# Performance work log

Hardware: AMD Instinct MI355X
Metric: run time of the kernel (lower is better)

Reference implementation:

```python
import jax, jax.numpy as jnp
import numpy as np

BATCH, SEQ, DMODEL, NSTATE = 4, 2048, 1024, 16


def setup_inputs() -> dict:
    key = jax.random.key(0)
    ks = jax.random.split(key, 6)
    def lin_w(k, out_d, in_d):
        # torch Linear default init scale ~ 1/sqrt(in_d)
        return jax.random.uniform(k, (out_d, in_d), jnp.float32, -1.0, 1.0) / np.sqrt(in_d).astype(np.float32)
    return {
        "x": jax.random.normal(ks[0], (BATCH, SEQ, DMODEL), jnp.float32),
        "W1": lin_w(ks[1], DMODEL, DMODEL), "b1": jnp.zeros((DMODEL,), jnp.float32),
        "W2": lin_w(ks[2], NSTATE, DMODEL), "b2": jnp.zeros((NSTATE,), jnp.float32),
        "W3": lin_w(ks[3], NSTATE, DMODEL), "b3": jnp.zeros((NSTATE,), jnp.float32),
        # A: xavier_uniform over (d_model, state_size)
        "A": jax.random.uniform(ks[4], (DMODEL, NSTATE), jnp.float32, -1.0, 1.0) * np.sqrt(6.0 / (DMODEL + NSTATE)).astype(np.float32),
    }


def reference(x, W1, b1, W2, b2, W3, b3, A):
    # Projections (bld -> bln / bld)
    Bmat = x @ W2.T + b2                      # (b, l, n)
    Cmat = x @ W3.T + b3                      # (b, l, n)
    delta = jax.nn.softplus(x @ W1.T + b1)    # (b, l, d)
    # Original math (flag=0 path):
    #   dB[b,l,d,n] = delta[b,l,d] * B[b,l,n]
    #   dA = exp(einsum('bld,dn->bldn', delta, A))  -- multiplied by a zeros h, so it
    #        contributes nothing to the output (dead math; A receives zero grad).
    #   h  = dA * 0 + x[...,None] * dB
    #   y  = einsum('bln,bldn->bld', C, h)
    # This reduces exactly to: y = x * delta * sum_n(B * C)
    bc = jnp.einsum('bln,bln->bl', Bmat, Cmat)  # (b, l)
    y = x * delta * bc[..., None]               # (b, l, d)
    return y
```

## Files before the change

kernel.cpp:

```cpp
#include <hip/hip_runtime.h>
#include <hip/hip_bf16.h>
#include <cmath>

#define BATCH 4
#define SEQ 2048
#define DM 1024
#define NS 16
#define M_ROWS (BATCH * SEQ)

typedef short bf16x8 __attribute__((ext_vector_type(8)));
typedef short bf16x4 __attribute__((ext_vector_type(4)));
typedef float f32x4 __attribute__((ext_vector_type(4)));

__device__ __forceinline__ short f2bf(float f) {
    union { float f; unsigned u; } a; a.f = f;
    unsigned u = a.u;
    return (short)((u + 0x7fffu + ((u >> 16) & 1u)) >> 16);
}
__device__ __forceinline__ float bf2f(unsigned short s) {
    union { unsigned u; float f; } a; a.u = ((unsigned)s) << 16;
    return a.f;
}

#define LDS_CAST(p) ((__attribute__((address_space(3))) unsigned*)(p))
#define GLB_CAST(p) ((const __attribute__((address_space(1))) unsigned*)(p))

__global__ void __launch_bounds__(256) convert_all(
    const float* __restrict__ x,  const float* __restrict__ W1,
    const float* __restrict__ W2, const float* __restrict__ W3,
    short* __restrict__ xb, short* __restrict__ W1b, short* __restrict__ Wcb)
{
    const int b = blockIdx.x;
    const int t = threadIdx.x;
    const float4* src; bf16x4* dst; int qbase;
    if (b < 2048)      { src = (const float4*)x;  dst = (bf16x4*)xb;  qbase = b * 1024; }
    else if (b < 2304) { src = (const float4*)W1; dst = (bf16x4*)W1b; qbase = (b - 2048) * 1024; }
    else if (b < 2308) { src = (const float4*)W2; dst = (bf16x4*)Wcb; qbase = (b - 2304) * 1024; }
    else               { src = (const float4*)W3; dst = (bf16x4*)(Wcb + NS * DM); qbase = (b - 2308) * 1024; }
    #pragma unroll
    for (int i = 0; i < 4; i++) {
        int q = qbase + i * 256 + t;
        float4 v = src[q];
        bf16x4 s;
        s.x = f2bf(v.x); s.y = f2bf(v.y); s.z = f2bf(v.z); s.w = f2bf(v.w);
        dst[q] = s;
    }
}

__global__ void __launch_bounds__(256) gemm_fused(
    const short* __restrict__ xb, const short* __restrict__ W1b,
    const short* __restrict__ Wcb, const float* __restrict__ b1,
    const float* __restrict__ b2,  const float* __restrict__ b3,
    float* __restrict__ out)
{
    __shared__ short As[64][64];
    __shared__ short Bs[128][64];
    __shared__ short Wcs[32][64];
    __shared__ float bcs[64];

    const int n0 = blockIdx.x * 128;
    const int m0 = blockIdx.y * 64;
    const int t = threadIdx.x;
    const int lane = t & 63;
    const int w = t >> 6;
    const int wm = (w >> 1) * 32;
    const int wn = (w & 1) * 64;
    const int lm = lane & 15;
    const int quad = lane >> 4;

    const int srow = t >> 3;
    const int schunk = t & 7;
    const int gch = (schunk ^ (srow & 7)) * 8;

    const short* pa0 = xb  + (size_t)(m0 + srow)      * DM + gch;
    const short* pa1 = xb  + (size_t)(m0 + 32 + srow) * DM + gch;
    const short* pb0 = W1b + (size_t)(n0 + srow)      * DM + gch;
    const short* pb1 = W1b + (size_t)(n0 + 32 + srow) * DM + gch;
    const short* pb2 = W1b + (size_t)(n0 + 64 + srow) * DM + gch;
    const short* pb3 = W1b + (size_t)(n0 + 96 + srow) * DM + gch;
    const short* pw  = Wcb + (size_t)srow             * DM + gch;

    f32x4 acc[2][4] = {};
    f32x4 abc[2] = {};

    #pragma unroll
    for (int kk = 0; kk < 16; kk++) {
        const int ke = kk * 64;
        __builtin_amdgcn_global_load_lds(GLB_CAST(pa0 + ke), LDS_CAST(&As[srow][schunk * 8]),      16, 0, 0);
        __builtin_amdgcn_global_load_lds(GLB_CAST(pa1 + ke), LDS_CAST(&As[32 + srow][schunk * 8]), 16, 0, 0);
        __builtin_amdgcn_global_load_lds(GLB_CAST(pb0 + ke), LDS_CAST(&Bs[srow][schunk * 8]),      16, 0, 0);
        __builtin_amdgcn_global_load_lds(GLB_CAST(pb1 + ke), LDS_CAST(&Bs[32 + srow][schunk * 8]), 16, 0, 0);
        __builtin_amdgcn_global_load_lds(GLB_CAST(pb2 + ke), LDS_CAST(&Bs[64 + srow][schunk * 8]), 16, 0, 0);
        __builtin_amdgcn_global_load_lds(GLB_CAST(pb3 + ke), LDS_CAST(&Bs[96 + srow][schunk * 8]), 16, 0, 0);
        __builtin_amdgcn_global_load_lds(GLB_CAST(pw  + ke), LDS_CAST(&Wcs[srow][schunk * 8]),     16, 0, 0);
        __syncthreads();

        #pragma unroll
        for (int ks = 0; ks < 2; ks++) {
            const int g = ks * 4 + quad;
            bf16x8 af[2], bfv[4], wcv[2], ab;
            #pragma unroll
            for (int i = 0; i < 2; i++) {
                int r = wm + i * 16 + lm;
                af[i] = *(const bf16x8*)&As[r][(g ^ (r & 7)) * 8];
            }
            #pragma unroll
            for (int j = 0; j < 4; j++) {
                int r = wn + j * 16 + lm;
                bfv[j] = *(const bf16x8*)&Bs[r][(g ^ (r & 7)) * 8];
            }
            {
                int rb = w * 16 + lm;
                ab = *(const bf16x8*)&As[rb][(g ^ (rb & 7)) * 8];
            }
            #pragma unroll
            for (int jj = 0; jj < 2; jj++) {
                int r = jj * 16 + lm;
                wcv[jj] = *(const bf16x8*)&Wcs[r][(g ^ (r & 7)) * 8];
            }
            #pragma unroll
            for (int i = 0; i < 2; i++)
                #pragma unroll
                for (int j = 0; j < 4; j++)
                    acc[i][j] = __builtin_amdgcn_mfma_f32_16x16x32_bf16(
                        af[i], bfv[j], acc[i][j], 0, 0, 0);
            #pragma unroll
            for (int jj = 0; jj < 2; jj++)
                abc[jj] = __builtin_amdgcn_mfma_f32_16x16x32_bf16(
                    ab, wcv[jj], abc[jj], 0, 0, 0);
        }
        __syncthreads();
    }

    float bb2 = b2[lm], bb3 = b3[lm];
    #pragma unroll
    for (int r = 0; r < 4; r++) {
        float p = (abc[0][r] + bb2) * (abc[1][r] + bb3);
        p += __shfl_xor(p, 1);
        p += __shfl_xor(p, 2);
        p += __shfl_xor(p, 4);
        p += __shfl_xor(p, 8);
        if (lm == 0) bcs[w * 16 + quad * 4 + r] = p;
    }
    __syncthreads();

    const unsigned short* xbu = (const unsigned short*)xb;
    float b1v[4];
    #pragma unroll
    for (int j = 0; j < 4; j++) b1v[j] = b1[n0 + wn + j * 16 + lm];

    #pragma unroll
    for (int i = 0; i < 2; i++) {
        #pragma unroll
        for (int r = 0; r < 4; r++) {
            int lrow = wm + i * 16 + quad * 4 + r;
            int gm = m0 + lrow;
            float bcv = bcs[lrow];
            const unsigned short* xrow = xbu + (size_t)gm * DM + n0 + wn + lm;
            float* orow = out + (size_t)gm * DM + n0 + wn + lm;
            #pragma unroll
            for (int j = 0; j < 4; j++) {
                float z = acc[i][j][r] + b1v[j];
                float az = __builtin_fabsf(z);
                float sp = fmaxf(z, 0.f) + __logf(1.f + __expf(-az));
                orow[j * 16] = bf2f(xrow[j * 16]) * sp * bcv;
            }
        }
    }
}

extern "C" void kernel_launch(void* const* d_in, const int* in_sizes, int n_in,
                              void* d_out, int out_size, void* d_ws, size_t ws_size,
                              hipStream_t stream) {
    const float* x  = (const float*)d_in[0];
    const float* W1 = (const float*)d_in[1];
    const float* b1 = (const float*)d_in[2];
    const float* W2 = (const float*)d_in[3];
    const float* b2 = (const float*)d_in[4];
    const float* W3 = (const float*)d_in[5];
    const float* b3 = (const float*)d_in[6];
    float* out = (float*)d_out;

    char* ws = (char*)d_ws;
    short* xb  = (short*)(ws);
    short* W1b = (short*)(ws + (size_t)16 * 1024 * 1024);
    short* Wcb = (short*)(ws + (size_t)18 * 1024 * 1024);

    convert_all<<<2312, 256, 0, stream>>>(x, W1, W2, W3, xb, W1b, Wcb);

    dim3 grid(DM / 128, M_ROWS / 64);
    gemm_fused<<<grid, 256, 0, stream>>>(xb, W1b, Wcb, b1, b2, b3, out);
}
```

Measured before the change: 128.0 us.

## Double-buffer LDS tiles with K=32 steps to overlap loads with MFMA

Splits the shared-memory tiles into two buffers of K=32 and prefetches the next K slice while MFMAs run on the current one, using a single barrier per iteration. The swizzle changes to a 4-chunk XOR pattern to match the narrower rows. The aim is to hide global-to-LDS latency behind compute. In exchange it doubles the number of iterations and barriers, and each barrier now waits on the in-flight prefetch, which may limit the overlap.

```diff
diff --git a/kernel.cpp b/kernel.cpp
--- a/kernel.cpp
+++ b/kernel.cpp
@@ -53,9 +53,9 @@
     const float* __restrict__ b2,  const float* __restrict__ b3,
     float* __restrict__ out)
 {
-    __shared__ short As[64][64];
-    __shared__ short Bs[128][64];
-    __shared__ short Wcs[32][64];
+    __shared__ short As[2][64][32];
+    __shared__ short Bs[2][128][32];
+    __shared__ short Wcs[2][32][32];
     __shared__ float bcs[64];
 
     const int n0 = blockIdx.x * 128;
@@ -68,67 +68,64 @@
     const int lm = lane & 15;
     const int quad = lane >> 4;
 
-    const int srow = t >> 3;
-    const int schunk = t & 7;
-    const int gch = (schunk ^ (srow & 7)) * 8;
+    const int srow = t >> 2;
+    const int sch  = t & 3;
+    const int gchS = (sch ^ (srow & 3)) * 8;
+    const int wrow = t >> 2;
+    const int gchW = (sch ^ (wrow & 3)) * 8;
 
-    const short* pa0 = xb  + (size_t)(m0 + srow)      * DM + gch;
-    const short* pa1 = xb  + (size_t)(m0 + 32 + srow) * DM + gch;
-    const short* pb0 = W1b + (size_t)(n0 + srow)      * DM + gch;
-    const short* pb1 = W1b + (size_t)(n0 + 32 + srow) * DM + gch;
-    const short* pb2 = W1b + (size_t)(n0 + 64 + srow) * DM + gch;
-    const short* pb3 = W1b + (size_t)(n0 + 96 + srow) * DM + gch;
-    const short* pw  = Wcb + (size_t)srow             * DM + gch;
+    const short* pa  = xb  + (size_t)(m0 + srow) * DM + gchS;
+    const short* pb0 = W1b + (size_t)(n0 + srow) * DM + gchS;
+    const short* pb1 = pb0 + (size_t)64 * DM;
+    const short* pw  = Wcb + (size_t)wrow * DM + gchW;
+
+    const int cs = ((quad ^ (lm & 3))) * 8;
 
     f32x4 acc[2][4] = {};
     f32x4 abc[2] = {};
 
+    __builtin_amdgcn_global_load_lds(GLB_CAST(pa),  LDS_CAST(&As[0][srow][sch * 8]),      16, 0, 0);
+    __builtin_amdgcn_global_load_lds(GLB_CAST(pb0), LDS_CAST(&Bs[0][srow][sch * 8]),      16, 0, 0);
+    __builtin_amdgcn_global_load_lds(GLB_CAST(pb1), LDS_CAST(&Bs[0][64 + srow][sch * 8]), 16, 0, 0);
+    if (t < 128)
+        __builtin_amdgcn_global_load_lds(GLB_CAST(pw), LDS_CAST(&Wcs[0][wrow][sch * 8]),  16, 0, 0);
+    __syncthreads();
+
     #pragma unroll
-    for (int kk = 0; kk < 16; kk++) {
-        const int ke = kk * 64;
-        __builtin_amdgcn_global_load_lds(GLB_CAST(pa0 + ke), LDS_CAST(&As[srow][schunk * 8]),      16, 0, 0);
-        __builtin_amdgcn_global_load_lds(GLB_CAST(pa1 + ke), LDS_CAST(&As[32 + srow][schunk * 8]), 16, 0, 0);
-        __builtin_amdgcn_global_load_lds(GLB_CAST(pb0 + ke), LDS_CAST(&Bs[srow][schunk * 8]),      16, 0, 0);
-        __builtin_amdgcn_global_load_lds(GLB_CAST(pb1 + ke), LDS_CAST(&Bs[32 + srow][schunk * 8]), 16, 0, 0);
-        __builtin_amdgcn_global_load_lds(GLB_CAST(pb2 + ke), LDS_CAST(&Bs[64 + srow][schunk * 8]), 16, 0, 0);
-        __builtin_amdgcn_global_load_lds(GLB_CAST(pb3 + ke), LDS_CAST(&Bs[96 + srow][schunk * 8]), 16, 0, 0);
-        __builtin_amdgcn_global_load_lds(GLB_CAST(pw  + ke), LDS_CAST(&Wcs[srow][schunk * 8]),     16, 0, 0);
-        __syncthreads();
+    for (int kk = 0; kk < 32; kk++) {
+        const int p = kk & 1;
+        if (kk < 31) {
+            const int ke = (kk + 1) * 32;
+            __builtin_amdgcn_global_load_lds(GLB_CAST(pa  + ke), LDS_CAST(&As[1 - p][srow][sch * 8]),      16, 0, 0);
+            __builtin_amdgcn_global_load_lds(GLB_CAST(pb0 + ke), LDS_CAST(&Bs[1 - p][srow][sch * 8]),      16, 0, 0);
+            __builtin_amdgcn_global_load_lds(GLB_CAST(pb1 + ke), LDS_CAST(&Bs[1 - p][64 + srow][sch * 8]), 16, 0, 0);
+            if (t < 128)
+                __builtin_amdgcn_global_load_lds(GLB_CAST(pw + ke), LDS_CAST(&Wcs[1 - p][wrow][sch * 8]),  16, 0, 0);
+        }
+
+        bf16x8 af[2], bfv[4], wcv[2], ab;
+        #pragma unroll
+        for (int i = 0; i < 2; i++)
+            af[i] = *(const bf16x8*)&As[p][wm + i * 16 + lm][cs];
+        #pragma unroll
+        for (int j = 0; j < 4; j++)
+            bfv[j] = *(const bf16x8*)&Bs[p][wn + j * 16 + lm][cs];
+        ab = *(const bf16x8*)&As[p][w * 16 + lm][cs];
+        #pragma unroll
+        for (int jj = 0; jj < 2; jj++)
+            wcv[jj] = *(const bf16x8*)&Wcs[p][jj * 16 + lm][cs];
 
         #pragma unroll
-        for (int ks = 0; ks < 2; ks++) {
-            const int g = ks * 4 + quad;
-            bf16x8 af[2], bfv[4], wcv[2], ab;
+        for (int i = 0; i < 2; i++)
             #pragma unroll
-            for (int i = 0; i < 2; i++) {
-                int r = wm + i * 16 + lm;
-                af[i] = *(const bf16x8*)&As[r][(g ^ (r & 7)) * 8];
-            }
-            #pragma unroll
-            for (int j = 0; j < 4; j++) {
-                int r = wn + j * 16 + lm;
-                bfv[j] = *(const bf16x8*)&Bs[r][(g ^ (r & 7)) * 8];
-            }
-            {
-                int rb = w * 16 + lm;
-                ab = *(const bf16x8*)&As[rb][(g ^ (rb & 7)) * 8];
-            }
-            #pragma unroll
-            for (int jj = 0; jj < 2; jj++) {
-                int r = jj * 16 + lm;
-                wcv[jj] = *(const bf16x8*)&Wcs[r][(g ^ (r & 7)) * 8];
-            }
-            #pragma unroll
-            for (int i = 0; i < 2; i++)
-                #pragma unroll
-                for (int j = 0; j < 4; j++)
-                    acc[i][j] = __builtin_amdgcn_mfma_f32_16x16x32_bf16(
-                        af[i], bfv[j], acc[i][j], 0, 0, 0);
-            #pragma unroll
-            for (int jj = 0; jj < 2; jj++)
-                abc[jj] = __builtin_amdgcn_mfma_f32_16x16x32_bf16(
-                    ab, wcv[jj], abc[jj], 0, 0, 0);
-        }
+            for (int j = 0; j < 4; j++)
+                acc[i][j] = __builtin_amdgcn_mfma_f32_16x16x32_bf16(
+                    af[i], bfv[j], acc[i][j], 0, 0, 0);
+        #pragma unroll
+        for (int jj = 0; jj < 2; jj++)
+            abc[jj] = __builtin_amdgcn_mfma_f32_16x16x32_bf16(
+                ab, wcv[jj], abc[jj], 0, 0, 0);
+
         __syncthreads();
     }
 
```

New measurement: 148.7 us. 1.16x slower.

## Enlarge GEMM tile to 128x128 with 4x4 MFMA fragments per wave

Applied to the files above, without the earlier changes.

Doubles the M tile from 64 to 128 rows, so each wave computes a 64x64 output region using 4x4 MFMA accumulators. The B/C projection now reuses the A fragments already loaded for the main GEMM instead of doing a separate LDS read. The goal is higher arithmetic intensity and less global and LDS traffic per output. In exchange there are more registers per thread, more LDS, and half as many blocks (512), which reduces occupancy and wave-level parallelism.

```diff
diff --git a/kernel.cpp b/kernel.cpp
--- a/kernel.cpp
+++ b/kernel.cpp
@@ -53,94 +53,88 @@
     const float* __restrict__ b2,  const float* __restrict__ b3,
     float* __restrict__ out)
 {
-    __shared__ short As[64][64];
+    __shared__ short As[128][64];
     __shared__ short Bs[128][64];
     __shared__ short Wcs[32][64];
-    __shared__ float bcs[64];
+    __shared__ float bcs[128];
 
     const int n0 = blockIdx.x * 128;
-    const int m0 = blockIdx.y * 64;
+    const int m0 = blockIdx.y * 128;
     const int t = threadIdx.x;
     const int lane = t & 63;
     const int w = t >> 6;
-    const int wm = (w >> 1) * 32;
+    const int wm = (w >> 1) * 64;
     const int wn = (w & 1) * 64;
     const int lm = lane & 15;
     const int quad = lane >> 4;
 
-    const int srow = t >> 3;
-    const int schunk = t & 7;
-    const int gch = (schunk ^ (srow & 7)) * 8;
+    const int sr  = t >> 3;
+    const int sc  = t & 7;
+    const int gch = (sc ^ (sr & 7)) * 8;
 
-    const short* pa0 = xb  + (size_t)(m0 + srow)      * DM + gch;
-    const short* pa1 = xb  + (size_t)(m0 + 32 + srow) * DM + gch;
-    const short* pb0 = W1b + (size_t)(n0 + srow)      * DM + gch;
-    const short* pb1 = W1b + (size_t)(n0 + 32 + srow) * DM + gch;
-    const short* pb2 = W1b + (size_t)(n0 + 64 + srow) * DM + gch;
-    const short* pb3 = W1b + (size_t)(n0 + 96 + srow) * DM + gch;
-    const short* pw  = Wcb + (size_t)srow             * DM + gch;
+    const short* pa = xb  + (size_t)(m0 + sr) * DM + gch;
+    const short* pb = W1b + (size_t)(n0 + sr) * DM + gch;
+    const short* pw = Wcb + (size_t)sr        * DM + gch;
 
-    f32x4 acc[2][4] = {};
-    f32x4 abc[2] = {};
+    f32x4 acc[4][4] = {};
+    f32x4 abc[2][2] = {};
 
     #pragma unroll
     for (int kk = 0; kk < 16; kk++) {
         const int ke = kk * 64;
-        __builtin_amdgcn_global_load_lds(GLB_CAST(pa0 + ke), LDS_CAST(&As[srow][schunk * 8]),      16, 0, 0);
-        __builtin_amdgcn_global_load_lds(GLB_CAST(pa1 + ke), LDS_CAST(&As[32 + srow][schunk * 8]), 16, 0, 0);
-        __builtin_amdgcn_global_load_lds(GLB_CAST(pb0 + ke), LDS_CAST(&Bs[srow][schunk * 8]),      16, 0, 0);
-        __builtin_amdgcn_global_load_lds(GLB_CAST(pb1 + ke), LDS_CAST(&Bs[32 + srow][schunk * 8]), 16, 0, 0);
-        __builtin_amdgcn_global_load_lds(GLB_CAST(pb2 + ke), LDS_CAST(&Bs[64 + srow][schunk * 8]), 16, 0, 0);
-        __builtin_amdgcn_global_load_lds(GLB_CAST(pb3 + ke), LDS_CAST(&Bs[96 + srow][schunk * 8]), 16, 0, 0);
-        __builtin_amdgcn_global_load_lds(GLB_CAST(pw  + ke), LDS_CAST(&Wcs[srow][schunk * 8]),     16, 0, 0);
+        #pragma unroll
+        for (int u = 0; u < 4; u++) {
+            __builtin_amdgcn_global_load_lds(GLB_CAST(pa + (size_t)u * 32 * DM + ke),
+                LDS_CAST(&As[u * 32 + sr][sc * 8]), 16, 0, 0);
+            __builtin_amdgcn_global_load_lds(GLB_CAST(pb + (size_t)u * 32 * DM + ke),
+                LDS_CAST(&Bs[u * 32 + sr][sc * 8]), 16, 0, 0);
+        }
+        __builtin_amdgcn_global_load_lds(GLB_CAST(pw + ke),
+            LDS_CAST(&Wcs[sr][sc * 8]), 16, 0, 0);
         __syncthreads();
 
         #pragma unroll
         for (int ks = 0; ks < 2; ks++) {
-            const int g = ks * 4 + quad;
-            bf16x8 af[2], bfv[4], wcv[2], ab;
+            const int cs = ((ks * 4 + quad) ^ (lm & 7)) * 8;
+            bf16x8 af[4], bfv[4], wcv[2];
             #pragma unroll
-            for (int i = 0; i < 2; i++) {
-                int r = wm + i * 16 + lm;
-                af[i] = *(const bf16x8*)&As[r][(g ^ (r & 7)) * 8];
-            }
+            for (int i = 0; i < 4; i++)
+                af[i] = *(const bf16x8*)&As[wm + i * 16 + lm][cs];
             #pragma unroll
-            for (int j = 0; j < 4; j++) {
-                int r = wn + j * 16 + lm;
-                bfv[j] = *(const bf16x8*)&Bs[r][(g ^ (r & 7)) * 8];
-            }
-            {
-                int rb = w * 16 + lm;
-                ab = *(const bf16x8*)&As[rb][(g ^ (rb & 7)) * 8];
-            }
+            for (int j = 0; j < 4; j++)
+                bfv[j] = *(const bf16x8*)&Bs[wn + j * 16 + lm][cs];
             #pragma unroll
-            for (int jj = 0; jj < 2; jj++) {
-                int r = jj * 16 + lm;
-                wcv[jj] = *(const bf16x8*)&Wcs[r][(g ^ (r & 7)) * 8];
-            }
+            for (int h = 0; h < 2; h++)
+                wcv[h] = *(const bf16x8*)&Wcs[h * 16 + lm][cs];
+
             #pragma unroll
-            for (int i = 0; i < 2; i++)
+            for (int i = 0; i < 4; i++)
                 #pragma unroll
                 for (int j = 0; j < 4; j++)
                     acc[i][j] = __builtin_amdgcn_mfma_f32_16x16x32_bf16(
                         af[i], bfv[j], acc[i][j], 0, 0, 0);
             #pragma unroll
-            for (int jj = 0; jj < 2; jj++)
-                abc[jj] = __builtin_amdgcn_mfma_f32_16x16x32_bf16(
-                    ab, wcv[jj], abc[jj], 0, 0, 0);
+            for (int i2 = 0; i2 < 2; i2++)
+                #pragma unroll
+                for (int h = 0; h < 2; h++)
+                    abc[i2][h] = __builtin_amdgcn_mfma_f32_16x16x32_bf16(
+                        af[(w & 1) * 2 + i2], wcv[h], abc[i2][h], 0, 0, 0);
         }
         __syncthreads();
     }
 
     float bb2 = b2[lm], bb3 = b3[lm];
     #pragma unroll
-    for (int r = 0; r < 4; r++) {
-        float p = (abc[0][r] + bb2) * (abc[1][r] + bb3);
-        p += __shfl_xor(p, 1);
-        p += __shfl_xor(p, 2);
-        p += __shfl_xor(p, 4);
-        p += __shfl_xor(p, 8);
-        if (lm == 0) bcs[w * 16 + quad * 4 + r] = p;
+    for (int i2 = 0; i2 < 2; i2++) {
+        #pragma unroll
+        for (int r = 0; r < 4; r++) {
+            float p = (abc[i2][0][r] + bb2) * (abc[i2][1][r] + bb3);
+            p += __shfl_xor(p, 1);
+            p += __shfl_xor(p, 2);
+            p += __shfl_xor(p, 4);
+            p += __shfl_xor(p, 8);
+            if (lm == 0) bcs[wm + (w & 1) * 32 + i2 * 16 + quad * 4 + r] = p;
+        }
     }
     __syncthreads();
 
@@ -150,7 +144,7 @@
     for (int j = 0; j < 4; j++) b1v[j] = b1[n0 + wn + j * 16 + lm];
 
     #pragma unroll
-    for (int i = 0; i < 2; i++) {
+    for (int i = 0; i < 4; i++) {
         #pragma unroll
         for (int r = 0; r < 4; r++) {
             int lrow = wm + i * 16 + quad * 4 + r;
@@ -188,6 +182,6 @@
 
     convert_all<<<2312, 256, 0, stream>>>(x, W1, W2, W3, xb, W1b, Wcb);
 
-    dim3 grid(DM / 128, M_ROWS / 64);
+    dim3 grid(DM / 128, M_ROWS / 128);
     gemm_fused<<<grid, 256, 0, stream>>>(xb, W1b, Wcb, b1, b2, b3, out);
 }
```

Result: slower. 481.0 us (+275.8%).
